# Performance work log

Hardware: AMD Instinct MI355X
Metric: run time of the kernel (lower is better)

## Reference

```python
import jax, jax.numpy as jnp
import numpy as np

R = 8            # receptive_field (hardcoded r=8 in GridProcessing call)
MARGIN = 0.6     # TripletLoss(margin=0.6)
EPS = 1e-8       # F.cosine_similarity eps


def _mine_cords(B, FH, FW):
    """Replicates GridProcessing._prepare for an identity flow field
    G[b, y, x] = ((x + 0.5) / W, (y + 0.5) / H):
    at every cell center, G_xmin = x, G_xmax = x + 1, both inside bounds, and
    [x // r, (x + 1) // r + 1) = {ix}, so the positive window collapses to the
    cell itself -> anchor_cord == positive_cord == (b, ix, iy) for every cell.
    (clip(0, 31) is benign since FH = FW = 32.)
    Negative cords from _prepare are discarded by forward(), so not produced."""
    bs, ys, xs = np.meshgrid(np.arange(B), np.arange(FH), np.arange(FW), indexing='ij')
    idx = np.stack([bs, xs, ys], axis=-1).reshape(-1, 3).astype(np.int32)  # rows: (b, x, y)
    return idx, idx.copy()


def setup_inputs() -> dict:
    key = jax.random.key(0)
    B, C, FH, FW = 16, 1024, 32, 32
    k1, k2 = jax.random.split(key)
    sketch = jax.random.normal(k1, (B, C, FH, FW), dtype=jnp.float32)
    ref = jax.random.normal(k2, (B, C, FH, FW), dtype=jnp.float32)
    a_idx, p_idx = _mine_cords(B, FH, FW)
    return {
        'sketch_query_vectors': sketch,
        'ref_key_vectors': ref,
        'anchor_idx': jnp.asarray(a_idx),
        'positive_idx': jnp.asarray(p_idx),
    }


def reference(sketch_query_vectors, ref_key_vectors, anchor_idx, positive_idx):
    B, C, FH, FW = sketch_query_vectors.shape
    HW = FH * FW
    N = anchor_idx.shape[0]
    na = N // B  # anchor rows are ordered by batch index, na anchors per image

    ax = anchor_idx[:, 1].reshape(B, na)
    ay = anchor_idx[:, 2].reshape(B, na)
    # anchor = sketch[b, :, y, x]  -> (B, na, C)
    a = sketch_query_vectors[jnp.arange(B)[:, None], :, ay, ax]

    # ref_fs.view(c, h*w).permute(1, 0): row-major flatten, flat id = y*W + x
    ref_flat = ref_key_vectors.reshape(B, C, HW).transpose(0, 2, 1)  # (B, HW, C)

    # cosine similarity of every anchor vs every ref position (per batch)
    dots = jnp.einsum('bnc,bmc->bnm', a, ref_flat)          # (B, na, HW)
    a_n = jnp.linalg.norm(a, axis=-1)                        # (B, na)
    r_n = jnp.linalg.norm(ref_flat, axis=-1)                 # (B, HW)
    sim = dots / jnp.maximum(a_n[:, :, None] * r_n[:, None, :], EPS)

    # get_negative_ids: argsort(dist)[:3] -> 3 LOWEST cosine positions;
    # loss uses sum of the 3 anchor-negative cosines (broadcasted cosine sum)
    neg_sum = -jnp.sum(jax.lax.top_k(-sim, 3)[0], axis=-1)   # (B, na)

    # cos(anchor, positive) is just sim at the positive's flat position
    pos_flat = (positive_idx[:, 2] * FW + positive_idx[:, 1]).reshape(B, na)
    cos_ap = jnp.take_along_axis(sim, pos_flat[:, :, None], axis=2)[..., 0]

    # (1 - cos_ap) - (1 - neg_sum) + margin, relu, mean over the single triplet
    losses = jax.nn.relu(neg_sum - cos_ap + MARGIN)          # (B, na)
    return jnp.sum(losses) / (1e-6 + N)
```

## Files before the change

kernel.cpp:

```cpp
#include <hip/hip_runtime.h>
#include <hip/hip_bf16.h>
#include <stdint.h>

#define BATCH 16
#define CDIM  1024
#define FWID  32
#define HW    1024
#define NA    1024
#define NTOT  (BATCH*NA)
#define NCHUNK 16
#define MARGIN 0.6f

typedef __bf16 bf16x8 __attribute__((ext_vector_type(8)));
typedef float  f32x4  __attribute__((ext_vector_type(4)));
typedef unsigned short us4 __attribute__((ext_vector_type(4)));
typedef unsigned short us8 __attribute__((ext_vector_type(8)));
typedef float  f4     __attribute__((ext_vector_type(4)));

template<int OFF>
__device__ __forceinline__ us4 tr_read(uint32_t addr){
  us4 r;
  asm volatile("ds_read_b64_tr_b16 %0, %1 offset:%2" : "=v"(r) : "v"(addr), "n"(OFF));
  return r;
}

__device__ __forceinline__ void gload16(const unsigned short* g, unsigned short* l){
  __builtin_amdgcn_global_load_lds((const __attribute__((address_space(1))) void*)g,
                                   (__attribute__((address_space(3))) void*)l, 16, 0, 0);
}

union FragU  { us4 h[2]; bf16x8 v; };
union FragU8 { us8 u;    bf16x8 v; };

__device__ __forceinline__ void ins3(float& a, float& b, float& c, float v){
  if (v < c){
    c = v;
    if (c < b){ float t=b; b=c; c=t;
      if (b < a){ t=a; a=b; b=t; }
    }
  }
}

#define MFMA __builtin_amdgcn_mfma_f32_16x16x32_bf16

__global__ __launch_bounds__(256)
void convert_transpose(const float* __restrict__ S, const float* __restrict__ R,
                       unsigned short* __restrict__ tS, unsigned short* __restrict__ tR,
                       float* __restrict__ pnorm){
  const int blk = blockIdx.x;
  const int e   = blk >> 11;
  const int b   = (blk >> 7) & 15;
  const int hwT = (blk >> 3) & 15;
  const int cT  = blk & 7;
  const float* src = (e ? R : S) + (size_t)b*CDIM*HW;
  unsigned short* dst = (e ? tR : tS) + (size_t)b*HW*CDIM;

  const int t   = threadIdx.x;
  const int cj  = t & 15;
  const int hwg = t >> 4;
  const int hw0 = hwT*64 + hwg*4;
  const int c0  = cT*128 + cj*8;

  f4 col[8];
  #pragma unroll
  for (int i = 0; i < 8; ++i)
    col[i] = *(const f4*)&src[(size_t)(c0 + i)*HW + hw0];

  float sq0=0.f, sq1=0.f, sq2=0.f, sq3=0.f;
  #pragma unroll
  for (int j = 0; j < 4; ++j){
    us8 pk;
    float sq = 0.f;
    #pragma unroll
    for (int i = 0; i < 8; ++i){
      __hip_bfloat16 h = __float2bfloat16(col[i][j]);
      pk[i] = __builtin_bit_cast(unsigned short, h);
      const float g = __bfloat162float(h);
      sq = fmaf(g, g, sq);
    }
    *(us8*)&dst[(size_t)(hw0 + j)*CDIM + c0] = pk;
    if (j==0) sq0=sq; else if (j==1) sq1=sq; else if (j==2) sq2=sq; else sq3=sq;
  }
  #pragma unroll
  for (int m = 1; m < 16; m <<= 1){
    sq0 += __shfl_xor(sq0, m);
    sq1 += __shfl_xor(sq1, m);
    sq2 += __shfl_xor(sq2, m);
    sq3 += __shfl_xor(sq3, m);
  }
  if (cj == 0){
    f4 o = {sq0, sq1, sq2, sq3};
    *(f4*)&pnorm[((size_t)(e*16 + b)*8 + cT)*HW + hw0] = o;
  }
}

__global__ __launch_bounds__(256)
void norm_reduce(const float* __restrict__ pnorm, float* __restrict__ snorm){
  const int eb = blockIdx.x;
  const int t  = threadIdx.x;
  #pragma unroll
  for (int r = 0; r < 4; ++r){
    const int hw = r*256 + t;
    float a = 0.f;
    #pragma unroll
    for (int ct = 0; ct < 8; ++ct)
      a += pnorm[((size_t)eb*8 + ct)*HW + hw];
    snorm[(size_t)eb*HW + hw] = sqrtf(a);
  }
}

__global__ __launch_bounds__(512, 2)
void fused_gemm_top3_v5(const unsigned short* __restrict__ tS,
                        const unsigned short* __restrict__ tR,
                        const float* __restrict__ snorm,
                        const int*   __restrict__ anchor,
                        const int*   __restrict__ posidx,
                        float* __restrict__ wtop,
                        float* __restrict__ wpos)
{
  __shared__ unsigned short stage[49152];
  __shared__ int   p_lds[256], q_lds[256];
  __shared__ float nAs[256], nBs[256];

  const int t = threadIdx.x;
  const uint32_t bid = blockIdx.x;
  const uint32_t L = (bid & 7u)*32u + (bid >> 3);
  const int b  = L >> 4;
  const int ni = (L >> 2) & 3;
  const int mi = L & 3;

  const unsigned short* SbT = tS + (size_t)b*HW*CDIM;
  const unsigned short* RbT = tR + (size_t)b*HW*CDIM;

  if (t < 256){
    const int n_g = ni*256 + t;
    const int* ap = anchor + (size_t)(b*NA + n_g)*3;
    const int* pp = posidx + (size_t)(b*NA + n_g)*3;
    const int pv = ap[2]*FWID + ap[1];
    p_lds[t] = pv;
    q_lds[t] = pp[2]*FWID + pp[1];
    nAs[t] = 1.0f / snorm[(size_t)b*HW + pv];
  } else {
    nBs[t-256] = 1.0f / snorm[(size_t)(BATCH + b)*HW + mi*256 + (t-256)];
  }
  __syncthreads();

  const int l  = t & 63;
  const int w  = t >> 6;
  const int wr = w >> 2, wc = w & 3;

  const int gkc = (l&3) ^ ((l>>3)&3);
  const int r0  = w*32 + (l>>2);
  const int r1  = r0 + 16;
  const unsigned short* gA0 = SbT + (size_t)p_lds[r0]*CDIM + gkc*8;
  const unsigned short* gA1 = SbT + (size_t)p_lds[r1]*CDIM + gkc*8;
  const unsigned short* gB0 = RbT + (size_t)(mi*256 + r0)*CDIM + gkc*8;
  const unsigned short* gB1 = RbT + (size_t)(mi*256 + r1)*CDIM + gkc*8;
  unsigned short* lA = &stage[w*1024];
  unsigned short* lB = &stage[24576 + w*1024];

  const int fbase = (l&15)*32 + (((l>>4) ^ ((l>>1)&3))*8);
  const int abase = wr*4096 + fbase;
  const int bbase = 24576 + wc*2048 + fbase;

  f32x4 acc[8][4];
  #pragma unroll
  for (int i=0;i<8;i++){
    #pragma unroll
    for (int j=0;j<4;j++){ f32x4 z = {0.f,0.f,0.f,0.f}; acc[i][j] = z; }
  }

  auto stage_fn = [&](int bo, int kt){
    const int ko = kt*32;
    gload16(gA0 + ko, lA + bo);
    gload16(gA1 + ko, lA + bo + 512);
    gload16(gB0 + ko, lB + bo);
    gload16(gB1 + ko, lB + bo + 512);
  };

  auto compute = [&](int bo){
    FragU8 Bf[4], Af[8];
    #pragma unroll
    for (int fb=0; fb<4; ++fb) Bf[fb].u = *(const us8*)&stage[bbase + bo + fb*512];
    #pragma unroll
    for (int fa=0; fa<8; ++fa) Af[fa].u = *(const us8*)&stage[abase + bo + fa*512];
    #pragma unroll
    for (int fa=0; fa<8; ++fa){
      #pragma unroll
      for (int fb=0; fb<4; ++fb)
        acc[fa][fb] = MFMA(Af[fa].v, Bf[fb].v, acc[fa][fb], 0,0,0);
    }
  };

  stage_fn(0, 0);
  stage_fn(8192, 1);
  int oc = 0, on = 8192, on2 = 16384;
  for (int kt = 0; kt < 32; ++kt){
    if (kt < 31) asm volatile("s_waitcnt vmcnt(4)" ::: "memory");
    else         asm volatile("s_waitcnt vmcnt(0)" ::: "memory");
    asm volatile("s_waitcnt lgkmcnt(0)" ::: "memory");
    __builtin_amdgcn_s_barrier();
    if (kt < 30) stage_fn(on2, kt+2);
    compute(oc);
    const int tmp = oc; oc = on; on = on2; on2 = tmp;
  }

  __syncthreads();

  float* tls = (float*)&stage[0] + (size_t)w*1152;

  float rinv[4];
  #pragma unroll
  for (int fb=0; fb<4; ++fb) rinv[fb] = nBs[wc*64 + fb*16 + (l&15)];

  #pragma unroll
  for (int fa=0; fa<8; ++fa){
    #pragma unroll
    for (int r=0; r<4; ++r){
      const int rg    = (l>>4)*4 + r;
      const int row_l = wr*128 + fa*16 + rg;
      const float ain = nAs[row_l];
      const float v0 = acc[fa][0][r] * ain * rinv[0];
      const float v1 = acc[fa][1][r] * ain * rinv[1];
      const float v2 = acc[fa][2][r] * ain * rinv[2];
      const float v3 = acc[fa][3][r] * ain * rinv[3];

      const int n_g = ni*256 + row_l;
      const int q   = q_lds[row_l];
      const int ql  = q - (mi*256 + wc*64);
      if (ql >= 0 && ql < 64 && (ql & 15) == (l & 15)){
        const int sel = ql >> 4;
        const float pv = sel==0 ? v0 : sel==1 ? v1 : sel==2 ? v2 : v3;
        wpos[b*NA + n_g] = pv;
      }

      float x=1e30f, y=1e30f, z=1e30f;
      ins3(x,y,z,v0); ins3(x,y,z,v1); ins3(x,y,z,v2); ins3(x,y,z,v3);
      f4 tr = {x, y, z, 0.f};
      *(f4*)(tls + (rg*17 + (l&15))*4) = tr;
    }
    asm volatile("s_waitcnt lgkmcnt(0)" ::: "memory");
    __builtin_amdgcn_sched_barrier(0);

    {
      const int rr = l >> 2;
      const float* rbp = tls + (rr*17 + (l&3)*4)*4;
      const f4 t0 = *(const f4*)(rbp);
      const f4 t1 = *(const f4*)(rbp + 4);
      const f4 t2 = *(const f4*)(rbp + 8);
      const f4 t3 = *(const f4*)(rbp + 12);
      float x = t0[0], y = t0[1], z = t0[2];
      ins3(x,y,z,t1[0]); ins3(x,y,z,t1[1]); ins3(x,y,z,t1[2]);
      ins3(x,y,z,t2[0]); ins3(x,y,z,t2[1]); ins3(x,y,z,t2[2]);
      ins3(x,y,z,t3[0]); ins3(x,y,z,t3[1]); ins3(x,y,z,t3[2]);
      #pragma unroll
      for (int m=1; m<4; m<<=1){
        const float ox = __shfl_xor(x, m);
        const float oy = __shfl_xor(y, m);
        const float oz = __shfl_xor(z, m);
        ins3(x,y,z,ox); ins3(x,y,z,oy); ins3(x,y,z,oz);
      }
      if ((l & 3) == 0){
        const int n_g = ni*256 + wr*128 + fa*16 + rr;
        float* dst = wtop + ((size_t)(b*NA + n_g)*NCHUNK + (mi*4 + wc))*3;
        dst[0]=x; dst[1]=y; dst[2]=z;
      }
    }
    asm volatile("s_waitcnt lgkmcnt(0)" ::: "memory");
    __builtin_amdgcn_sched_barrier(0);
  }
}

__global__ __launch_bounds__(256)
void fused_gemm_top3_v1(const float* __restrict__ sketch,
                        const float* __restrict__ refk,
                        const int*   __restrict__ anchor,
                        const int*   __restrict__ posidx,
                        float* __restrict__ wtop,
                        float* __restrict__ wpos)
{
  __shared__ union {
    unsigned short stage[16384];
    struct { float nA[16][128]; float nB[16][128]; } nrm;
  } sh;
  __shared__ int   p_lds[128];
  __shared__ float nA2[128], nB2[128];

  const int t = threadIdx.x;
  const uint32_t bid = blockIdx.x;
  const uint32_t L = (bid & 7u)*128u + (bid >> 3);
  const int b  = L >> 6;
  const int ni = (L >> 3) & 7;
  const int mi = L & 7;

  const float* Sb = sketch + (size_t)b*CDIM*HW;
  const float* Rb = refk   + (size_t)b*CDIM*HW;

  if (t < 128){
    const int n_g = ni*128 + t;
    const int* ap = anchor + (size_t)(b*NA + n_g)*3;
    p_lds[t] = ap[2]*FWID + ap[1];
  }
  __syncthreads();
  const int p0 = p_lds[0];
  int okf = 1;
  if (t < 128) okf = (p_lds[t] == p0 + t);
  const int contig = __syncthreads_and(okf);

  const int colg = (t & 15)*8;
  const int rowg = t >> 4;
  const int mbase = mi*128;

  const int l  = t & 63;
  const int w  = t >> 6;
  const int wr = w >> 1, wc = w & 1;
  const uint32_t sh_base = (uint32_t)(uintptr_t)&sh.stage[0];
  const uint32_t laneA = ((uint32_t)(l>>4))*2048u + (uint32_t)wr*512u + (uint32_t)(l&15)*8u;
  const uint32_t laneB = ((uint32_t)(l>>4))*2048u + (uint32_t)wc*512u + (uint32_t)(l&15)*8u;
  const int off0 = ((rowg>>2)*8 + (colg>>4))*64 + (rowg&3)*16 + (colg&15);

  f32x4 acc[4][4];
  #pragma unroll
  for (int i=0;i<4;i++){
    #pragma unroll
    for (int j=0;j<4;j++){ f32x4 z = {0.f,0.f,0.f,0.f}; acc[i][j] = z; }
  }

  float sqA[8] = {0,0,0,0,0,0,0,0};
  float sqB[8] = {0,0,0,0,0,0,0,0};
  f4 ra[4], rb[4];

  auto load_tile = [&](int kt){
    const int c0 = kt*32 + rowg;
    const float* SA = Sb + (size_t)c0*HW;
    const float* RB = Rb + (size_t)c0*HW + mbase + colg;
    if (contig){
      const float* pA = SA + p0 + colg;
      ra[0] = *(const f4*)(pA);
      ra[1] = *(const f4*)(pA + 4);
      ra[2] = *(const f4*)(pA + 16*HW);
      ra[3] = *(const f4*)(pA + 16*HW + 4);
    } else {
      float* raf = (float*)ra;
      #pragma unroll
      for (int i=0;i<8;i++){
        const int pc = p_lds[colg + i];
        raf[i]   = SA[pc];
        raf[8+i] = SA[16*HW + pc];
      }
    }
    rb[0] = *(const f4*)(RB);
    rb[1] = *(const f4*)(RB + 4);
    rb[2] = *(const f4*)(RB + 16*HW);
    rb[3] = *(const f4*)(RB + 16*HW + 4);
  };

  auto cvt_store = [&](int buf){
    const float* raf = (const float*)ra;
    const float* rbf = (const float*)rb;
    us8 pk;
    #pragma unroll
    for (int i=0;i<8;i++){
      __hip_bfloat16 h = __float2bfloat16(raf[i]);
      pk[i] = __builtin_bit_cast(unsigned short, h);
      const float g = __bfloat162float(h);
      sqA[i] = fmaf(g, g, sqA[i]);
    }
    *(us8*)&sh.stage[buf*4096 + off0] = pk;
    #pragma unroll
    for (int i=0;i<8;i++){
      __hip_bfloat16 h = __float2bfloat16(raf[8+i]);
      pk[i] = __builtin_bit_cast(unsigned short, h);
      const float g = __bfloat162float(h);
      sqA[i] = fmaf(g, g, sqA[i]);
    }
    *(us8*)&sh.stage[buf*4096 + off0 + 2048] = pk;
    #pragma unroll
    for (int i=0;i<8;i++){
      __hip_bfloat16 h = __float2bfloat16(rbf[i]);
      pk[i] = __builtin_bit_cast(unsigned short, h);
      const float g = __bfloat162float(h);
      sqB[i] = fmaf(g, g, sqB[i]);
    }
    *(us8*)&sh.stage[8192 + buf*4096 + off0] = pk;
    #pragma unroll
    for (int i=0;i<8;i++){
      __hip_bfloat16 h = __float2bfloat16(rbf[8+i]);
      pk[i] = __builtin_bit_cast(unsigned short, h);
      const float g = __bfloat162float(h);
      sqB[i] = fmaf(g, g, sqB[i]);
    }
    *(us8*)&sh.stage[8192 + buf*4096 + off0 + 2048] = pk;
  };

  auto compute = [&](int buf){
    const uint32_t aaddr = sh_base + (uint32_t)buf*8192u + laneA;
    const uint32_t baddr = sh_base + 16384u + (uint32_t)buf*8192u + laneB;
    FragU A0,A1,A2,A3,B0,B1,B2,B3;
    A0.h[0]=tr_read<0>(aaddr);    A0.h[1]=tr_read<1024>(aaddr);
    A1.h[0]=tr_read<128>(aaddr);  A1.h[1]=tr_read<1152>(aaddr);
    A2.h[0]=tr_read<256>(aaddr);  A2.h[1]=tr_read<1280>(aaddr);
    A3.h[0]=tr_read<384>(aaddr);  A3.h[1]=tr_read<1408>(aaddr);
    B0.h[0]=tr_read<0>(baddr);    B0.h[1]=tr_read<1024>(baddr);
    B1.h[0]=tr_read<128>(baddr);  B1.h[1]=tr_read<1152>(baddr);
    B2.h[0]=tr_read<256>(baddr);  B2.h[1]=tr_read<1280>(baddr);
    B3.h[0]=tr_read<384>(baddr);  B3.h[1]=tr_read<1408>(baddr);
    asm volatile("s_waitcnt lgkmcnt(0)" ::: "memory");
    __builtin_amdgcn_sched_barrier(0);
    acc[0][0]=MFMA(A0.v,B0.v,acc[0][0],0,0,0);
    acc[0][1]=MFMA(A0.v,B1.v,acc[0][1],0,0,0);
    acc[0][2]=MFMA(A0.v,B2.v,acc[0][2],0,0,0);
    acc[0][3]=MFMA(A0.v,B3.v,acc[0][3],0,0,0);
    acc[1][0]=MFMA(A1.v,B0.v,acc[1][0],0,0,0);
    acc[1][1]=MFMA(A1.v,B1.v,acc[1][1],0,0,0);
    acc[1][2]=MFMA(A1.v,B2.v,acc[1][2],0,0,0);
    acc[1][3]=MFMA(A1.v,B3.v,acc[1][3],0,0,0);
    acc[2][0]=MFMA(A2.v,B0.v,acc[2][0],0,0,0);
    acc[2][1]=MFMA(A2.v,B1.v,acc[2][1],0,0,0);
    acc[2][2]=MFMA(A2.v,B2.v,acc[2][2],0,0,0);
    acc[2][3]=MFMA(A2.v,B3.v,acc[2][3],0,0,0);
    acc[3][0]=MFMA(A3.v,B0.v,acc[3][0],0,0,0);
    acc[3][1]=MFMA(A3.v,B1.v,acc[3][1],0,0,0);
    acc[3][2]=MFMA(A3.v,B2.v,acc[3][2],0,0,0);
    acc[3][3]=MFMA(A3.v,B3.v,acc[3][3],0,0,0);
  };

  load_tile(0);
  cvt_store(0);
  __syncthreads();
  int buf = 0;
  for (int kt = 0; kt < 32; ++kt){
    if (kt < 31) load_tile(kt+1);
    compute(buf);
    if (kt < 31) cvt_store(buf^1);
    __syncthreads();
    buf ^= 1;
  }

  #pragma unroll
  for (int i=0;i<8;i++) sh.nrm.nA[rowg][colg+i] = sqA[i];
  #pragma unroll
  for (int i=0;i<8;i++) sh.nrm.nB[rowg][colg+i] = sqB[i];
  __syncthreads();
  if (t < 128){
    float s = 0.f;
    #pragma unroll
    for (int r=0;r<16;r++) s += sh.nrm.nA[r][t];
    nA2[t] = s;
  } else {
    const int c2 = t - 128;
    float s = 0.f;
    #pragma unroll
    for (int r=0;r<16;r++) s += sh.nrm.nB[r][c2];
    nB2[c2] = s;
  }
  __syncthreads();

  float rncol[4];
  #pragma unroll
  for (int nf=0;nf<4;nf++) rncol[nf] = sqrtf(nB2[wc*64 + nf*16 + (l&15)]);

  #pragma unroll
  for (int mf=0; mf<4; ++mf){
    #pragma unroll
    for (int r=0; r<4; ++r){
      const int row_l = wr*64 + mf*16 + (l>>4)*4 + r;
      const int n_g   = ni*128 + row_l;
      const float an  = sqrtf(nA2[row_l]);
      const float v0 = acc[mf][0][r] / fmaxf(an*rncol[0], 1e-8f);
      const float v1 = acc[mf][1][r] / fmaxf(an*rncol[1], 1e-8f);
      const float v2 = acc[mf][2][r] / fmaxf(an*rncol[2], 1e-8f);
      const float v3 = acc[mf][3][r] / fmaxf(an*rncol[3], 1e-8f);

      const int* pp = posidx + (size_t)(b*NA + n_g)*3;
      const int q  = pp[2]*FWID + pp[1];
      const int ql = q - (mbase + wc*64);
      if (ql >= 0 && ql < 64 && (ql & 15) == (l & 15)){
        const int sel = ql >> 4;
        const float pv = sel==0 ? v0 : sel==1 ? v1 : sel==2 ? v2 : v3;
        wpos[b*NA + n_g] = pv;
      }

      float x=1e30f, y=1e30f, z=1e30f;
      ins3(x,y,z,v0); ins3(x,y,z,v1); ins3(x,y,z,v2); ins3(x,y,z,v3);
      #pragma unroll
      for (int m=1; m<16; m<<=1){
        const float ox = __shfl_xor(x, m);
        const float oy = __shfl_xor(y, m);
        const float oz = __shfl_xor(z, m);
        ins3(x,y,z,ox); ins3(x,y,z,oy); ins3(x,y,z,oz);
      }
      if ((l & 15) == 0){
        float* dst = wtop + ((size_t)(b*NA + n_g)*NCHUNK + (mi*2 + wc))*3;
        dst[0]=x; dst[1]=y; dst[2]=z;
      }
    }
  }
}

__global__ __launch_bounds__(256)
void merge_top3(const float* __restrict__ wtop, const float* __restrict__ wpos,
                float* __restrict__ partial){
  __shared__ float red[256];
  const int id = blockIdx.x*256 + threadIdx.x;
  const float* src = wtop + (size_t)id*(NCHUNK*3);
  float x=1e30f, y=1e30f, z=1e30f;
  #pragma unroll
  for (int i=0;i<NCHUNK*3;i++) ins3(x,y,z, src[i]);
  const float loss = fmaxf((x+y+z) - wpos[id] + MARGIN, 0.0f);
  red[threadIdx.x] = loss;
  __syncthreads();
  for (int s=128; s>0; s>>=1){
    if (threadIdx.x < s) red[threadIdx.x] += red[threadIdx.x+s];
    __syncthreads();
  }
  if (threadIdx.x == 0) partial[blockIdx.x] = red[0];
}

__global__ void final_sum(const float* __restrict__ partial, float* __restrict__ out){
  float v = partial[threadIdx.x];
  #pragma unroll
  for (int off=32; off>0; off>>=1) v += __shfl_down(v, off);
  if (threadIdx.x == 0) out[0] = v / (1e-6f + (float)NTOT);
}

extern "C" void kernel_launch(void* const* d_in, const int* in_sizes, int n_in,
                              void* d_out, int out_size, void* d_ws, size_t ws_size,
                              hipStream_t stream){
  const float* sketch = (const float*)d_in[0];
  const float* refk   = (const float*)d_in[1];
  const int*   anchor = (const int*)d_in[2];
  const int*   posidx = (const int*)d_in[3];
  float* out = (float*)d_out;

  float* wtop    = (float*)d_ws;
  float* wpos    = wtop + (size_t)NTOT*NCHUNK*3;
  float* partial = wpos + NTOT;
  unsigned short* tS = (unsigned short*)(partial + 256);
  unsigned short* tR = tS + (size_t)BATCH*HW*CDIM;
  float* pnorm = (float*)(tR + (size_t)BATCH*HW*CDIM);
  float* snorm = pnorm + (size_t)32*8*1024;
  const size_t need = (size_t)((char*)(snorm + 32*1024) - (char*)d_ws);

  if (ws_size >= need){
    convert_transpose<<<dim3(4096), dim3(256), 0, stream>>>(sketch, refk, tS, tR, pnorm);
    norm_reduce<<<dim3(32), dim3(256), 0, stream>>>(pnorm, snorm);
    fused_gemm_top3_v5<<<dim3(256), dim3(512), 0, stream>>>(tS, tR, snorm, anchor, posidx, wtop, wpos);
  } else {
    fused_gemm_top3_v1<<<dim3(1024), dim3(256), 0, stream>>>(sketch, refk, anchor, posidx, wtop, wpos);
  }
  merge_top3<<<dim3(64), dim3(256), 0, stream>>>(wtop, wpos, partial);
  final_sum<<<dim3(1), dim3(64), 0, stream>>>(partial, out);
}
```

Before: 104.4 us.

## Stage transpose through LDS for coalesced writes and shrink GEMM tiles to 128x128

The convert/transpose kernel now packs bf16 values into an LDS tile and writes full 64-byte contiguous row segments, instead of scattered 16-byte stores. Per-position squared norms are reduced through LDS rather than warp shuffles. The fused GEMM+top3 kernel moves from 256x256 tiles with 512 threads (256 blocks) to 128x128 tiles with 256 threads (1024 blocks), targeting 3 blocks per CU. This gives more parallelism and occupancy on 256 CUs at the cost of less operand reuse per block and more global traffic.

```diff
diff --git a/kernel.cpp b/kernel.cpp
--- a/kernel.cpp
+++ b/kernel.cpp
@@ -44,9 +44,12 @@
 #define MFMA __builtin_amdgcn_mfma_f32_16x16x32_bf16
 
 __global__ __launch_bounds__(256)
-void convert_transpose(const float* __restrict__ S, const float* __restrict__ R,
-                       unsigned short* __restrict__ tS, unsigned short* __restrict__ tR,
-                       float* __restrict__ pnorm){
+void convert_transpose2(const float* __restrict__ S, const float* __restrict__ R,
+                        unsigned short* __restrict__ tS, unsigned short* __restrict__ tR,
+                        float* __restrict__ pnorm){
+  __shared__ unsigned short tile[64*136];
+  __shared__ float nsq[64][17];
+
   const int blk = blockIdx.x;
   const int e   = blk >> 11;
   const int b   = (blk >> 7) & 15;
@@ -55,42 +58,58 @@
   const float* src = (e ? R : S) + (size_t)b*CDIM*HW;
   unsigned short* dst = (e ? tR : tS) + (size_t)b*HW*CDIM;
 
-  const int t   = threadIdx.x;
-  const int cj  = t & 15;
-  const int hwg = t >> 4;
-  const int hw0 = hwT*64 + hwg*4;
-  const int c0  = cT*128 + cj*8;
-
-  f4 col[8];
-  #pragma unroll
-  for (int i = 0; i < 8; ++i)
-    col[i] = *(const f4*)&src[(size_t)(c0 + i)*HW + hw0];
-
+  const int t  = threadIdx.x;
+  const int gi = t >> 4;
+  const int li = t & 15;
+  const int hwb = hwT*64 + li*4;
+
+  us8 hj0, hj1, hj2, hj3;
   float sq0=0.f, sq1=0.f, sq2=0.f, sq3=0.f;
   #pragma unroll
-  for (int j = 0; j < 4; ++j){
-    us8 pk;
-    float sq = 0.f;
-    #pragma unroll
-    for (int i = 0; i < 8; ++i){
-      __hip_bfloat16 h = __float2bfloat16(col[i][j]);
-      pk[i] = __builtin_bit_cast(unsigned short, h);
-      const float g = __bfloat162float(h);
-      sq = fmaf(g, g, sq);
-    }
-    *(us8*)&dst[(size_t)(hw0 + j)*CDIM + c0] = pk;
-    if (j==0) sq0=sq; else if (j==1) sq1=sq; else if (j==2) sq2=sq; else sq3=sq;
-  }
-  #pragma unroll
-  for (int m = 1; m < 16; m <<= 1){
-    sq0 += __shfl_xor(sq0, m);
-    sq1 += __shfl_xor(sq1, m);
-    sq2 += __shfl_xor(sq2, m);
-    sq3 += __shfl_xor(sq3, m);
-  }
-  if (cj == 0){
-    f4 o = {sq0, sq1, sq2, sq3};
-    *(f4*)&pnorm[((size_t)(e*16 + b)*8 + cT)*HW + hw0] = o;
+  for (int i = 0; i < 8; ++i){
+    const int c = cT*128 + gi*8 + i;
+    const f4 v = *(const f4*)&src[(size_t)c*HW + hwb];
+    __hip_bfloat16 h0 = __float2bfloat16(v[0]);
+    __hip_bfloat16 h1 = __float2bfloat16(v[1]);
+    __hip_bfloat16 h2 = __float2bfloat16(v[2]);
+    __hip_bfloat16 h3 = __float2bfloat16(v[3]);
+    hj0[i] = __builtin_bit_cast(unsigned short, h0);
+    hj1[i] = __builtin_bit_cast(unsigned short, h1);
+    hj2[i] = __builtin_bit_cast(unsigned short, h2);
+    hj3[i] = __builtin_bit_cast(unsigned short, h3);
+    const float g0 = __bfloat162float(h0), g1 = __bfloat162float(h1);
+    const float g2 = __bfloat162float(h2), g3 = __bfloat162float(h3);
+    sq0 = fmaf(g0,g0,sq0); sq1 = fmaf(g1,g1,sq1);
+    sq2 = fmaf(g2,g2,sq2); sq3 = fmaf(g3,g3,sq3);
+  }
+  *(us8*)&tile[(li*4+0)*136 + gi*8] = hj0;
+  *(us8*)&tile[(li*4+1)*136 + gi*8] = hj1;
+  *(us8*)&tile[(li*4+2)*136 + gi*8] = hj2;
+  *(us8*)&tile[(li*4+3)*136 + gi*8] = hj3;
+  nsq[li*4+0][gi] = sq0;
+  nsq[li*4+1][gi] = sq1;
+  nsq[li*4+2][gi] = sq2;
+  nsq[li*4+3][gi] = sq3;
+  __syncthreads();
+
+  const int hw_l = t >> 2;
+  const int cg   = t & 3;
+  const unsigned short* row = &tile[hw_l*136 + cg*32];
+  const us8 o0 = *(const us8*)(row);
+  const us8 o1 = *(const us8*)(row + 8);
+  const us8 o2 = *(const us8*)(row + 16);
+  const us8 o3 = *(const us8*)(row + 24);
+  unsigned short* drow = dst + (size_t)(hwT*64 + hw_l)*CDIM + cT*128 + cg*32;
+  *(us8*)(drow)      = o0;
+  *(us8*)(drow + 8)  = o1;
+  *(us8*)(drow + 16) = o2;
+  *(us8*)(drow + 24) = o3;
+
+  if (t < 64){
+    float a = 0.f;
+    #pragma unroll
+    for (int g = 0; g < 16; ++g) a += nsq[t][g];
+    pnorm[((size_t)(e*16 + b)*8 + cT)*HW + hwT*64 + t] = a;
   }
 }
 
@@ -109,8 +128,8 @@
   }
 }
 
-__global__ __launch_bounds__(512, 2)
-void fused_gemm_top3_v5(const unsigned short* __restrict__ tS,
+__global__ __launch_bounds__(256, 3)
+void fused_gemm_top3_v6(const unsigned short* __restrict__ tS,
                         const unsigned short* __restrict__ tR,
                         const float* __restrict__ snorm,
                         const int*   __restrict__ anchor,
@@ -118,22 +137,22 @@
                         float* __restrict__ wtop,
                         float* __restrict__ wpos)
 {
-  __shared__ unsigned short stage[49152];
-  __shared__ int   p_lds[256], q_lds[256];
-  __shared__ float nAs[256], nBs[256];
+  __shared__ unsigned short stage[24576];
+  __shared__ int   p_lds[128], q_lds[128];
+  __shared__ float nAs[128], nBs[128];
 
   const int t = threadIdx.x;
   const uint32_t bid = blockIdx.x;
-  const uint32_t L = (bid & 7u)*32u + (bid >> 3);
-  const int b  = L >> 4;
-  const int ni = (L >> 2) & 3;
-  const int mi = L & 3;
+  const uint32_t L = (bid & 7u)*128u + (bid >> 3);
+  const int b  = L >> 6;
+  const int ni = (L >> 3) & 7;
+  const int mi = L & 7;
 
   const unsigned short* SbT = tS + (size_t)b*HW*CDIM;
   const unsigned short* RbT = tR + (size_t)b*HW*CDIM;
 
-  if (t < 256){
-    const int n_g = ni*256 + t;
+  if (t < 128){
+    const int n_g = ni*128 + t;
     const int* ap = anchor + (size_t)(b*NA + n_g)*3;
     const int* pp = posidx + (size_t)(b*NA + n_g)*3;
     const int pv = ap[2]*FWID + ap[1];
@@ -141,31 +160,31 @@
     q_lds[t] = pp[2]*FWID + pp[1];
     nAs[t] = 1.0f / snorm[(size_t)b*HW + pv];
   } else {
-    nBs[t-256] = 1.0f / snorm[(size_t)(BATCH + b)*HW + mi*256 + (t-256)];
+    nBs[t-128] = 1.0f / snorm[(size_t)(BATCH + b)*HW + mi*128 + (t-128)];
   }
   __syncthreads();
 
   const int l  = t & 63;
   const int w  = t >> 6;
-  const int wr = w >> 2, wc = w & 3;
+  const int wr = w >> 1, wc = w & 1;
 
   const int gkc = (l&3) ^ ((l>>3)&3);
   const int r0  = w*32 + (l>>2);
   const int r1  = r0 + 16;
   const unsigned short* gA0 = SbT + (size_t)p_lds[r0]*CDIM + gkc*8;
   const unsigned short* gA1 = SbT + (size_t)p_lds[r1]*CDIM + gkc*8;
-  const unsigned short* gB0 = RbT + (size_t)(mi*256 + r0)*CDIM + gkc*8;
-  const unsigned short* gB1 = RbT + (size_t)(mi*256 + r1)*CDIM + gkc*8;
+  const unsigned short* gB0 = RbT + (size_t)(mi*128 + r0)*CDIM + gkc*8;
+  const unsigned short* gB1 = RbT + (size_t)(mi*128 + r1)*CDIM + gkc*8;
   unsigned short* lA = &stage[w*1024];
-  unsigned short* lB = &stage[24576 + w*1024];
+  unsigned short* lB = &stage[12288 + w*1024];
 
   const int fbase = (l&15)*32 + (((l>>4) ^ ((l>>1)&3))*8);
-  const int abase = wr*4096 + fbase;
-  const int bbase = 24576 + wc*2048 + fbase;
-
-  f32x4 acc[8][4];
-  #pragma unroll
-  for (int i=0;i<8;i++){
+  const int abase = wr*2048 + fbase;
+  const int bbase = 12288 + wc*2048 + fbase;
+
+  f32x4 acc[4][4];
+  #pragma unroll
+  for (int i=0;i<4;i++){
     #pragma unroll
     for (int j=0;j<4;j++){ f32x4 z = {0.f,0.f,0.f,0.f}; acc[i][j] = z; }
   }
@@ -179,13 +198,13 @@
   };
 
   auto compute = [&](int bo){
-    FragU8 Bf[4], Af[8];
+    FragU8 Bf[4], Af[4];
     #pragma unroll
     for (int fb=0; fb<4; ++fb) Bf[fb].u = *(const us8*)&stage[bbase + bo + fb*512];
     #pragma unroll
-    for (int fa=0; fa<8; ++fa) Af[fa].u = *(const us8*)&stage[abase + bo + fa*512];
-    #pragma unroll
-    for (int fa=0; fa<8; ++fa){
+    for (int fa=0; fa<4; ++fa) Af[fa].u = *(const us8*)&stage[abase + bo + fa*512];
+    #pragma unroll
+    for (int fa=0; fa<4; ++fa){
       #pragma unroll
       for (int fb=0; fb<4; ++fb)
         acc[fa][fb] = MFMA(Af[fa].v, Bf[fb].v, acc[fa][fb], 0,0,0);
@@ -193,8 +212,8 @@
   };
 
   stage_fn(0, 0);
-  stage_fn(8192, 1);
-  int oc = 0, on = 8192, on2 = 16384;
+  stage_fn(4096, 1);
+  int oc = 0, on = 4096, on2 = 8192;
   for (int kt = 0; kt < 32; ++kt){
     if (kt < 31) asm volatile("s_waitcnt vmcnt(4)" ::: "memory");
     else         asm volatile("s_waitcnt vmcnt(0)" ::: "memory");
@@ -206,7 +225,6 @@
   }
 
   __syncthreads();
-
   float* tls = (float*)&stage[0] + (size_t)w*1152;
 
   float rinv[4];
@@ -214,20 +232,20 @@
   for (int fb=0; fb<4; ++fb) rinv[fb] = nBs[wc*64 + fb*16 + (l&15)];
 
   #pragma unroll
-  for (int fa=0; fa<8; ++fa){
+  for (int fa=0; fa<4; ++fa){
     #pragma unroll
     for (int r=0; r<4; ++r){
       const int rg    = (l>>4)*4 + r;
-      const int row_l = wr*128 + fa*16 + rg;
+      const int row_l = wr*64 + fa*16 + rg;
       const float ain = nAs[row_l];
       const float v0 = acc[fa][0][r] * ain * rinv[0];
       const float v1 = acc[fa][1][r] * ain * rinv[1];
       const float v2 = acc[fa][2][r] * ain * rinv[2];
       const float v3 = acc[fa][3][r] * ain * rinv[3];
 
-      const int n_g = ni*256 + row_l;
+      const int n_g = ni*128 + row_l;
       const int q   = q_lds[row_l];
-      const int ql  = q - (mi*256 + wc*64);
+      const int ql  = q - (mi*128 + wc*64);
       if (ql >= 0 && ql < 64 && (ql & 15) == (l & 15)){
         const int sel = ql >> 4;
         const float pv = sel==0 ? v0 : sel==1 ? v1 : sel==2 ? v2 : v3;
@@ -261,8 +279,8 @@
         ins3(x,y,z,ox); ins3(x,y,z,oy); ins3(x,y,z,oz);
       }
       if ((l & 3) == 0){
-        const int n_g = ni*256 + wr*128 + fa*16 + rr;
-        float* dst = wtop + ((size_t)(b*NA + n_g)*NCHUNK + (mi*4 + wc))*3;
+        const int n_g = ni*128 + wr*64 + fa*16 + rr;
+        float* dst = wtop + ((size_t)(b*NA + n_g)*NCHUNK + (mi*2 + wc))*3;
         dst[0]=x; dst[1]=y; dst[2]=z;
       }
     }
@@ -543,9 +561,9 @@
   const size_t need = (size_t)((char*)(snorm + 32*1024) - (char*)d_ws);
 
   if (ws_size >= need){
-    convert_transpose<<<dim3(4096), dim3(256), 0, stream>>>(sketch, refk, tS, tR, pnorm);
+    convert_transpose2<<<dim3(4096), dim3(256), 0, stream>>>(sketch, refk, tS, tR, pnorm);
     norm_reduce<<<dim3(32), dim3(256), 0, stream>>>(pnorm, snorm);
-    fused_gemm_top3_v5<<<dim3(256), dim3(512), 0, stream>>>(tS, tR, snorm, anchor, posidx, wtop, wpos);
+    fused_gemm_top3_v6<<<dim3(1024), dim3(256), 0, stream>>>(tS, tR, snorm, anchor, posidx, wtop, wpos);
   } else {
     fused_gemm_top3_v1<<<dim3(1024), dim3(256), 0, stream>>>(sketch, refk, anchor, posidx, wtop, wpos);
   }
```

Measured after the change: 113.8 us. 1.09x slower.

## Split GEMM main loop into two interleaved halves with staggered prefetch and priority

Applied to the files above, without the earlier changes.

Restructures the triple-buffered bf16 MFMA main loop so A and B global-to-LDS prefetches are issued at different points in the iteration, and the 8x4 MFMA block is split into two 4x4 halves with their LDS fragment loads interleaved. It raises wave priority around MFMA bursts with s_setprio and pins the order with sched_barrier. The aim is to overlap LDS reads and global loads with matrix math and cut stalls at the per-iteration barrier. It adds a second barrier per iteration and hand-tuned vmcnt counts that must match the new load ordering.

```diff
diff --git a/kernel.cpp b/kernel.cpp
--- a/kernel.cpp
+++ b/kernel.cpp
@@ -110,7 +110,7 @@
 }
 
 __global__ __launch_bounds__(512, 2)
-void fused_gemm_top3_v5(const unsigned short* __restrict__ tS,
+void fused_gemm_top3_v7(const unsigned short* __restrict__ tS,
                         const unsigned short* __restrict__ tR,
                         const float* __restrict__ snorm,
                         const int*   __restrict__ anchor,
@@ -170,43 +170,90 @@
     for (int j=0;j<4;j++){ f32x4 z = {0.f,0.f,0.f,0.f}; acc[i][j] = z; }
   }
 
-  auto stage_fn = [&](int bo, int kt){
+  auto stageA = [&](int bo, int kt){
     const int ko = kt*32;
     gload16(gA0 + ko, lA + bo);
     gload16(gA1 + ko, lA + bo + 512);
+  };
+  auto stageB = [&](int bo, int kt){
+    const int ko = kt*32;
     gload16(gB0 + ko, lB + bo);
     gload16(gB1 + ko, lB + bo + 512);
   };
 
-  auto compute = [&](int bo){
-    FragU8 Bf[4], Af[8];
-    #pragma unroll
-    for (int fb=0; fb<4; ++fb) Bf[fb].u = *(const us8*)&stage[bbase + bo + fb*512];
-    #pragma unroll
-    for (int fa=0; fa<8; ++fa) Af[fa].u = *(const us8*)&stage[abase + bo + fa*512];
-    #pragma unroll
-    for (int fa=0; fa<8; ++fa){
-      #pragma unroll
-      for (int fb=0; fb<4; ++fb)
-        acc[fa][fb] = MFMA(Af[fa].v, Bf[fb].v, acc[fa][fb], 0,0,0);
-    }
-  };
-
-  stage_fn(0, 0);
-  stage_fn(8192, 1);
+  stageA(0, 0);     stageB(0, 0);
+  stageA(8192, 1);  stageB(8192, 1);
+
   int oc = 0, on = 8192, on2 = 16384;
   for (int kt = 0; kt < 32; ++kt){
-    if (kt < 31) asm volatile("s_waitcnt vmcnt(4)" ::: "memory");
-    else         asm volatile("s_waitcnt vmcnt(0)" ::: "memory");
+    if (kt < 30) stageA(on2, kt+2);
+    if (kt < 30)       { asm volatile("s_waitcnt vmcnt(6)" ::: "memory"); }
+    else if (kt == 30) { asm volatile("s_waitcnt vmcnt(4)" ::: "memory"); }
+    else               { asm volatile("s_waitcnt vmcnt(0)" ::: "memory"); }
+    __builtin_amdgcn_s_barrier();
+
+    FragU8 Bf0,Bf1,Bf2,Bf3, Af0,Af1,Af2,Af3;
+    Bf0.u = *(const us8*)&stage[bbase + oc];
+    Bf1.u = *(const us8*)&stage[bbase + oc + 512];
+    Bf2.u = *(const us8*)&stage[bbase + oc + 1024];
+    Bf3.u = *(const us8*)&stage[bbase + oc + 1536];
+    Af0.u = *(const us8*)&stage[abase + oc];
+    Af1.u = *(const us8*)&stage[abase + oc + 512];
+    Af2.u = *(const us8*)&stage[abase + oc + 1024];
+    Af3.u = *(const us8*)&stage[abase + oc + 1536];
     asm volatile("s_waitcnt lgkmcnt(0)" ::: "memory");
+    __builtin_amdgcn_sched_barrier(0);
+    __builtin_amdgcn_s_setprio(1);
+    acc[0][0]=MFMA(Af0.v,Bf0.v,acc[0][0],0,0,0);
+    acc[0][1]=MFMA(Af0.v,Bf1.v,acc[0][1],0,0,0);
+    acc[0][2]=MFMA(Af0.v,Bf2.v,acc[0][2],0,0,0);
+    acc[0][3]=MFMA(Af0.v,Bf3.v,acc[0][3],0,0,0);
+    acc[1][0]=MFMA(Af1.v,Bf0.v,acc[1][0],0,0,0);
+    acc[1][1]=MFMA(Af1.v,Bf1.v,acc[1][1],0,0,0);
+    acc[1][2]=MFMA(Af1.v,Bf2.v,acc[1][2],0,0,0);
+    acc[1][3]=MFMA(Af1.v,Bf3.v,acc[1][3],0,0,0);
+    acc[2][0]=MFMA(Af2.v,Bf0.v,acc[2][0],0,0,0);
+    acc[2][1]=MFMA(Af2.v,Bf1.v,acc[2][1],0,0,0);
+    acc[2][2]=MFMA(Af2.v,Bf2.v,acc[2][2],0,0,0);
+    acc[2][3]=MFMA(Af2.v,Bf3.v,acc[2][3],0,0,0);
+    acc[3][0]=MFMA(Af3.v,Bf0.v,acc[3][0],0,0,0);
+    acc[3][1]=MFMA(Af3.v,Bf1.v,acc[3][1],0,0,0);
+    acc[3][2]=MFMA(Af3.v,Bf2.v,acc[3][2],0,0,0);
+    acc[3][3]=MFMA(Af3.v,Bf3.v,acc[3][3],0,0,0);
+    __builtin_amdgcn_s_setprio(0);
+
+    if (kt < 30) stageB(on2, kt+2);
+    FragU8 Ag0,Ag1,Ag2,Ag3;
+    Ag0.u = *(const us8*)&stage[abase + oc + 2048];
+    Ag1.u = *(const us8*)&stage[abase + oc + 2560];
+    Ag2.u = *(const us8*)&stage[abase + oc + 3072];
+    Ag3.u = *(const us8*)&stage[abase + oc + 3584];
+    asm volatile("s_waitcnt lgkmcnt(0)" ::: "memory");
+    __builtin_amdgcn_sched_barrier(0);
+    __builtin_amdgcn_s_setprio(1);
+    acc[4][0]=MFMA(Ag0.v,Bf0.v,acc[4][0],0,0,0);
+    acc[4][1]=MFMA(Ag0.v,Bf1.v,acc[4][1],0,0,0);
+    acc[4][2]=MFMA(Ag0.v,Bf2.v,acc[4][2],0,0,0);
+    acc[4][3]=MFMA(Ag0.v,Bf3.v,acc[4][3],0,0,0);
+    acc[5][0]=MFMA(Ag1.v,Bf0.v,acc[5][0],0,0,0);
+    acc[5][1]=MFMA(Ag1.v,Bf1.v,acc[5][1],0,0,0);
+    acc[5][2]=MFMA(Ag1.v,Bf2.v,acc[5][2],0,0,0);
+    acc[5][3]=MFMA(Ag1.v,Bf3.v,acc[5][3],0,0,0);
+    acc[6][0]=MFMA(Ag2.v,Bf0.v,acc[6][0],0,0,0);
+    acc[6][1]=MFMA(Ag2.v,Bf1.v,acc[6][1],0,0,0);
+    acc[6][2]=MFMA(Ag2.v,Bf2.v,acc[6][2],0,0,0);
+    acc[6][3]=MFMA(Ag2.v,Bf3.v,acc[6][3],0,0,0);
+    acc[7][0]=MFMA(Ag3.v,Bf0.v,acc[7][0],0,0,0);
+    acc[7][1]=MFMA(Ag3.v,Bf1.v,acc[7][1],0,0,0);
+    acc[7][2]=MFMA(Ag3.v,Bf2.v,acc[7][2],0,0,0);
+    acc[7][3]=MFMA(Ag3.v,Bf3.v,acc[7][3],0,0,0);
+    __builtin_amdgcn_s_setprio(0);
     __builtin_amdgcn_s_barrier();
-    if (kt < 30) stage_fn(on2, kt+2);
-    compute(oc);
+
     const int tmp = oc; oc = on; on = on2; on2 = tmp;
   }
 
   __syncthreads();
-
   float* tls = (float*)&stage[0] + (size_t)w*1152;
 
   float rinv[4];
@@ -545,7 +592,7 @@
   if (ws_size >= need){
     convert_transpose<<<dim3(4096), dim3(256), 0, stream>>>(sketch, refk, tS, tR, pnorm);
     norm_reduce<<<dim3(32), dim3(256), 0, stream>>>(pnorm, snorm);
-    fused_gemm_top3_v5<<<dim3(256), dim3(512), 0, stream>>>(tS, tR, snorm, anchor, posidx, wtop, wpos);
+    fused_gemm_top3_v7<<<dim3(256), dim3(512), 0, stream>>>(tS, tR, snorm, anchor, posidx, wtop, wpos);
   } else {
     fused_gemm_top3_v1<<<dim3(1024), dim3(256), 0, stream>>>(sketch, refk, anchor, posidx, wtop, wpos);
   }
```

Result: faster. 101.7 us (-2.6%).

## Software-pipeline LDS fragment reads with MFMA in GEMM main loop

Applied to the files above, without the earlier changes.

Restructures the bf16 GEMM K-loop so fragment reads from shared memory for the next K-tile, plus the upper-half A fragments, are issued while MFMAs on the current tile run. It double-buffers register fragments, splits each tile's MFMA work into two halves around the barrier, and adds sched_barrier and setprio hints. The goal is to hide LDS read latency and barrier stalls behind matrix work. The cost is more live registers, which may hurt occupancy under launch_bounds(512,2), and a more intricate, fragile schedule.

```diff
diff --git a/kernel.cpp b/kernel.cpp
--- a/kernel.cpp
+++ b/kernel.cpp
@@ -110,7 +110,7 @@
 }
 
 __global__ __launch_bounds__(512, 2)
-void fused_gemm_top3_v5(const unsigned short* __restrict__ tS,
+void fused_gemm_top3_v8(const unsigned short* __restrict__ tS,
                         const unsigned short* __restrict__ tR,
                         const float* __restrict__ snorm,
                         const int*   __restrict__ anchor,
@@ -170,7 +170,7 @@
     for (int j=0;j<4;j++){ f32x4 z = {0.f,0.f,0.f,0.f}; acc[i][j] = z; }
   }
 
-  auto stage_fn = [&](int bo, int kt){
+  auto stage4 = [&](int bo, int kt){
     const int ko = kt*32;
     gload16(gA0 + ko, lA + bo);
     gload16(gA1 + ko, lA + bo + 512);
@@ -178,35 +178,136 @@
     gload16(gB1 + ko, lB + bo + 512);
   };
 
-  auto compute = [&](int bo){
-    FragU8 Bf[4], Af[8];
-    #pragma unroll
-    for (int fb=0; fb<4; ++fb) Bf[fb].u = *(const us8*)&stage[bbase + bo + fb*512];
-    #pragma unroll
-    for (int fa=0; fa<8; ++fa) Af[fa].u = *(const us8*)&stage[abase + bo + fa*512];
-    #pragma unroll
-    for (int fa=0; fa<8; ++fa){
-      #pragma unroll
-      for (int fb=0; fb<4; ++fb)
-        acc[fa][fb] = MFMA(Af[fa].v, Bf[fb].v, acc[fa][fb], 0,0,0);
-    }
+  FragU8 Bc0,Bc1,Bc2,Bc3, Bn0,Bn1,Bn2,Bn3;
+  FragU8 Ac0,Ac1,Ac2,Ac3, An0,An1,An2,An3;
+  FragU8 Ah0,Ah1,Ah2,Ah3;
+
+#define RD(dst, off) (dst).u = *(const us8*)&stage[(off)]
+
+  auto mfma_lo = [&](FragU8& A0, FragU8& A1, FragU8& A2, FragU8& A3,
+                     FragU8& B0, FragU8& B1, FragU8& B2, FragU8& B3){
+    acc[0][0]=MFMA(A0.v,B0.v,acc[0][0],0,0,0);
+    acc[0][1]=MFMA(A0.v,B1.v,acc[0][1],0,0,0);
+    acc[0][2]=MFMA(A0.v,B2.v,acc[0][2],0,0,0);
+    acc[0][3]=MFMA(A0.v,B3.v,acc[0][3],0,0,0);
+    acc[1][0]=MFMA(A1.v,B0.v,acc[1][0],0,0,0);
+    acc[1][1]=MFMA(A1.v,B1.v,acc[1][1],0,0,0);
+    acc[1][2]=MFMA(A1.v,B2.v,acc[1][2],0,0,0);
+    acc[1][3]=MFMA(A1.v,B3.v,acc[1][3],0,0,0);
+    acc[2][0]=MFMA(A2.v,B0.v,acc[2][0],0,0,0);
+    acc[2][1]=MFMA(A2.v,B1.v,acc[2][1],0,0,0);
+    acc[2][2]=MFMA(A2.v,B2.v,acc[2][2],0,0,0);
+    acc[2][3]=MFMA(A2.v,B3.v,acc[2][3],0,0,0);
+    acc[3][0]=MFMA(A3.v,B0.v,acc[3][0],0,0,0);
+    acc[3][1]=MFMA(A3.v,B1.v,acc[3][1],0,0,0);
+    acc[3][2]=MFMA(A3.v,B2.v,acc[3][2],0,0,0);
+    acc[3][3]=MFMA(A3.v,B3.v,acc[3][3],0,0,0);
   };
-
-  stage_fn(0, 0);
-  stage_fn(8192, 1);
+  auto mfma_hi = [&](FragU8& B0, FragU8& B1, FragU8& B2, FragU8& B3){
+    acc[4][0]=MFMA(Ah0.v,B0.v,acc[4][0],0,0,0);
+    acc[4][1]=MFMA(Ah0.v,B1.v,acc[4][1],0,0,0);
+    acc[4][2]=MFMA(Ah0.v,B2.v,acc[4][2],0,0,0);
+    acc[4][3]=MFMA(Ah0.v,B3.v,acc[4][3],0,0,0);
+    acc[5][0]=MFMA(Ah1.v,B0.v,acc[5][0],0,0,0);
+    acc[5][1]=MFMA(Ah1.v,B1.v,acc[5][1],0,0,0);
+    acc[5][2]=MFMA(Ah1.v,B2.v,acc[5][2],0,0,0);
+    acc[5][3]=MFMA(Ah1.v,B3.v,acc[5][3],0,0,0);
+    acc[6][0]=MFMA(Ah2.v,B0.v,acc[6][0],0,0,0);
+    acc[6][1]=MFMA(Ah2.v,B1.v,acc[6][1],0,0,0);
+    acc[6][2]=MFMA(Ah2.v,B2.v,acc[6][2],0,0,0);
+    acc[6][3]=MFMA(Ah2.v,B3.v,acc[6][3],0,0,0);
+    acc[7][0]=MFMA(Ah3.v,B0.v,acc[7][0],0,0,0);
+    acc[7][1]=MFMA(Ah3.v,B1.v,acc[7][1],0,0,0);
+    acc[7][2]=MFMA(Ah3.v,B2.v,acc[7][2],0,0,0);
+    acc[7][3]=MFMA(Ah3.v,B3.v,acc[7][3],0,0,0);
+  };
+
+#define RD_AHI(OC) \
+  RD(Ah0, abase + (OC) + 2048); RD(Ah1, abase + (OC) + 2560); \
+  RD(Ah2, abase + (OC) + 3072); RD(Ah3, abase + (OC) + 3584)
+
+#define RD_SET(B0,B1,B2,B3,A0,A1,A2,A3, OFF) \
+  RD(B0, bbase + (OFF));        RD(B1, bbase + (OFF) + 512); \
+  RD(B2, bbase + (OFF) + 1024); RD(B3, bbase + (OFF) + 1536); \
+  RD(A0, abase + (OFF));        RD(A1, abase + (OFF) + 512); \
+  RD(A2, abase + (OFF) + 1024); RD(A3, abase + (OFF) + 1536)
+
+  stage4(0, 0);
+  stage4(8192, 1);
+  asm volatile("s_waitcnt vmcnt(4)" ::: "memory");
+  __builtin_amdgcn_s_barrier();
+  __builtin_amdgcn_sched_barrier(0);
+  RD_SET(Bc0,Bc1,Bc2,Bc3, Ac0,Ac1,Ac2,Ac3, 0);
+
   int oc = 0, on = 8192, on2 = 16384;
-  for (int kt = 0; kt < 32; ++kt){
-    if (kt < 31) asm volatile("s_waitcnt vmcnt(4)" ::: "memory");
-    else         asm volatile("s_waitcnt vmcnt(0)" ::: "memory");
+  for (int kt2 = 0; kt2 < 15; ++kt2){
+    const int kt = 2*kt2;
+    stage4(on2, kt+2);
+    RD_AHI(oc);
+    __builtin_amdgcn_sched_barrier(0);
+    __builtin_amdgcn_s_setprio(1);
+    mfma_lo(Ac0,Ac1,Ac2,Ac3, Bc0,Bc1,Bc2,Bc3);
+    __builtin_amdgcn_s_setprio(0);
     asm volatile("s_waitcnt lgkmcnt(0)" ::: "memory");
+    asm volatile("s_waitcnt vmcnt(4)" ::: "memory");
     __builtin_amdgcn_s_barrier();
-    if (kt < 30) stage_fn(on2, kt+2);
-    compute(oc);
-    const int tmp = oc; oc = on; on = on2; on2 = tmp;
-  }
+    __builtin_amdgcn_sched_barrier(0);
+    RD_SET(Bn0,Bn1,Bn2,Bn3, An0,An1,An2,An3, on);
+    __builtin_amdgcn_sched_barrier(0);
+    __builtin_amdgcn_s_setprio(1);
+    mfma_hi(Bc0,Bc1,Bc2,Bc3);
+    __builtin_amdgcn_s_setprio(0);
+    { const int tmp = oc; oc = on; on = on2; on2 = tmp; }
+
+    stage4(on2, kt+3);
+    RD_AHI(oc);
+    __builtin_amdgcn_sched_barrier(0);
+    __builtin_amdgcn_s_setprio(1);
+    mfma_lo(An0,An1,An2,An3, Bn0,Bn1,Bn2,Bn3);
+    __builtin_amdgcn_s_setprio(0);
+    asm volatile("s_waitcnt lgkmcnt(0)" ::: "memory");
+    asm volatile("s_waitcnt vmcnt(4)" ::: "memory");
+    __builtin_amdgcn_s_barrier();
+    __builtin_amdgcn_sched_barrier(0);
+    RD_SET(Bc0,Bc1,Bc2,Bc3, Ac0,Ac1,Ac2,Ac3, on);
+    __builtin_amdgcn_sched_barrier(0);
+    __builtin_amdgcn_s_setprio(1);
+    mfma_hi(Bn0,Bn1,Bn2,Bn3);
+    __builtin_amdgcn_s_setprio(0);
+    { const int tmp = oc; oc = on; on = on2; on2 = tmp; }
+  }
+
+  RD_AHI(oc);
+  __builtin_amdgcn_sched_barrier(0);
+  __builtin_amdgcn_s_setprio(1);
+  mfma_lo(Ac0,Ac1,Ac2,Ac3, Bc0,Bc1,Bc2,Bc3);
+  __builtin_amdgcn_s_setprio(0);
+  asm volatile("s_waitcnt lgkmcnt(0)" ::: "memory");
+  asm volatile("s_waitcnt vmcnt(0)" ::: "memory");
+  __builtin_amdgcn_s_barrier();
+  __builtin_amdgcn_sched_barrier(0);
+  RD_SET(Bn0,Bn1,Bn2,Bn3, An0,An1,An2,An3, on);
+  __builtin_amdgcn_sched_barrier(0);
+  __builtin_amdgcn_s_setprio(1);
+  mfma_hi(Bc0,Bc1,Bc2,Bc3);
+  __builtin_amdgcn_s_setprio(0);
+  { const int tmp = oc; oc = on; on = on2; on2 = tmp; }
+
+  RD_AHI(oc);
+  __builtin_amdgcn_sched_barrier(0);
+  __builtin_amdgcn_s_setprio(1);
+  mfma_lo(An0,An1,An2,An3, Bn0,Bn1,Bn2,Bn3);
+  __builtin_amdgcn_s_setprio(0);
+  asm volatile("s_waitcnt lgkmcnt(0)" ::: "memory");
+  __builtin_amdgcn_s_setprio(1);
+  mfma_hi(Bn0,Bn1,Bn2,Bn3);
+  __builtin_amdgcn_s_setprio(0);
+
+#undef RD
+#undef RD_AHI
+#undef RD_SET
 
   __syncthreads();
-
   float* tls = (float*)&stage[0] + (size_t)w*1152;
 
   float rinv[4];
@@ -545,7 +646,7 @@
   if (ws_size >= need){
     convert_transpose<<<dim3(4096), dim3(256), 0, stream>>>(sketch, refk, tS, tR, pnorm);
     norm_reduce<<<dim3(32), dim3(256), 0, stream>>>(pnorm, snorm);
-    fused_gemm_top3_v5<<<dim3(256), dim3(512), 0, stream>>>(tS, tR, snorm, anchor, posidx, wtop, wpos);
+    fused_gemm_top3_v8<<<dim3(256), dim3(512), 0, stream>>>(tS, tR, snorm, anchor, posidx, wtop, wpos);
   } else {
     fused_gemm_top3_v1<<<dim3(1024), dim3(256), 0, stream>>>(sketch, refk, anchor, posidx, wtop, wpos);
   }
```

After: 99.38 us. -4.8%, faster.
